# Optimization experiments

Hardware: AMD Instinct MI355X
Metric: run time of the kernel (lower is better)

The kernel has to match this reference:

```python
import jax, jax.numpy as jnp
import numpy as np

N = 8192      # nodes; also input feature dim (x.shape[0] used as in_channels)
E = 524288    # edges per edge type (avg degree 64)
H = 200       # hidden dim (hard-coded in RecomNet)
MEAN_RATING = 3.5


def setup_inputs() -> dict:
    key = jax.random.key(0)
    ks = jax.random.split(key, 14)
    s_in = np.float32(1.0 / np.sqrt(N))
    s_h = np.float32(1.0 / np.sqrt(H))
    return {
        "x": jax.random.normal(ks[0], (N, N), jnp.float32),
        "edge_sim": jax.random.randint(ks[1], (2, E), 0, N),
        "edge_rat": jax.random.randint(ks[2], (2, E), 0, N),
        "mask": jax.random.randint(ks[3], (E,), 0, 2).astype(bool),
        # conv1 params (in=N, out=H)
        "w1_self": jax.random.normal(ks[4], (N, H), jnp.float32) * s_in,
        "w1_sim": jax.random.normal(ks[5], (N, H), jnp.float32) * s_in,
        "w1_rat": jax.random.normal(ks[6], (N, H), jnp.float32) * s_in,
        "b1": jnp.zeros((H,), jnp.float32),
        # conv2 params (in=H, out=H)
        "w2_self": jax.random.normal(ks[7], (H, H), jnp.float32) * s_h,
        "w2_sim": jax.random.normal(ks[8], (H, H), jnp.float32) * s_h,
        "w2_rat": jax.random.normal(ks[9], (H, H), jnp.float32) * s_h,
        "b2": jnp.zeros((H,), jnp.float32),
        # bilinear decoder
        "Q": jax.random.normal(ks[10], (H, H), jnp.float32) * s_h,
    }


def _recom_conv(edge_sim, edge_rat, x, w_self, w_sim, w_rat, b):
    # linear-then-gather-then-scatter (linear commutes with sum aggregation)
    m_sim = (x @ w_sim)[edge_sim[0]]                                   # [E, H]
    agg_sim = jax.ops.segment_sum(m_sim, edge_sim[1], num_segments=N)  # [N, H]
    m_rat = (x @ w_rat)[edge_rat[0]]
    agg_rat = jax.ops.segment_sum(m_rat, edge_rat[1], num_segments=N)
    return x @ w_self + agg_sim + agg_rat + b


def reference(x, w1_self, w1_sim, w1_rat, b1, w2_self, w2_sim, w2_rat, b2, Q,
              edge_sim, edge_rat, mask):
    h = _recom_conv(edge_sim, edge_rat, x, w1_self, w1_sim, w1_rat, b1)
    h = jax.nn.relu(h)
    h = _recom_conv(edge_sim, edge_rat, h, w2_self, w2_sim, w2_rat, b2)
    h1 = h[edge_rat[0]]                                                # [E, H]
    h2 = h[edge_rat[1]]                                                # [E, H]
    pred = jnp.einsum("eh,hk,ek->e", h1, Q, h2) + MEAN_RATING          # [E]
    # original compacts with boolean mask (dynamic shape); here we keep a
    # fixed [E] output and zero out unmasked edges
    return jnp.where(mask, pred, 0.0)
```

## Files before the change

### kernel.cpp

```cpp
#include <hip/hip_runtime.h>

#define NN 8192
#define EE 524288
#define HPAD 256
#define NP 640
#define PSS ((size_t)NN * 200)
#define PSM ((size_t)NN * 400)

using s16x8 = __attribute__((ext_vector_type(8))) short;
using u16x8 = __attribute__((ext_vector_type(8))) unsigned short;
using f32x4 = __attribute__((ext_vector_type(4))) float;

__device__ __forceinline__ unsigned short f2b(float f) {
    unsigned u = __float_as_uint(f);
    u = (u + 0x7FFFu + ((u >> 16) & 1u)) >> 16;
    return (unsigned short)u;
}
__device__ __forceinline__ float b2f(unsigned short u) {
    return __uint_as_float((unsigned)u << 16);
}

__device__ __forceinline__ void async16(const unsigned short* g, unsigned short* l)
{
    __builtin_amdgcn_global_load_lds(
        (const __attribute__((address_space(1))) unsigned int*)g,
        (__attribute__((address_space(3))) unsigned int*)l, 16, 0, 0);
}


__global__ void cvt_f2b_kernel(const float* __restrict__ in,
                               unsigned short* __restrict__ out, int n8)
{
    int i = blockIdx.x * 256 + threadIdx.x;
    if (i >= n8) return;
    float4 v0 = ((const float4*)in)[2 * i];
    float4 v1 = ((const float4*)in)[2 * i + 1];
    u16x8 o;
    o[0] = f2b(v0.x); o[1] = f2b(v0.y); o[2] = f2b(v0.z); o[3] = f2b(v0.w);
    o[4] = f2b(v1.x); o[5] = f2b(v1.y); o[6] = f2b(v1.z); o[7] = f2b(v1.w);
    ((u16x8*)out)[i] = o;
}

__global__ void transpose_w_kernel(
    const float* __restrict__ u0, const float* __restrict__ u1,
    const float* __restrict__ u2,
    const float* __restrict__ v0, const float* __restrict__ v1,
    const float* __restrict__ v2,
    const float* __restrict__ Q,
    unsigned short* __restrict__ o0, unsigned short* __restrict__ o1,
    unsigned short* __restrict__ o2)
{
    const int zc = blockIdx.z;
    const float *w0, *w1, *w2;
    unsigned short* out;
    int Kout, Kreal, Nreal;
    if (zc == 0)      { w0 = u0; w1 = u1; w2 = u2; out = o0; Kout = NN;   Kreal = NN;  Nreal = 600; }
    else if (zc == 1) { w0 = v0; w1 = v1; w2 = v2; out = o1; Kout = HPAD; Kreal = 200; Nreal = 600; }
    else              { w0 = Q;  w1 = Q;  w2 = Q;  out = o2; Kout = HPAD; Kreal = 200; Nreal = 200; }
    const int kb = blockIdx.x << 5;
    const int nb = blockIdx.y << 5;
    if (kb >= Kout) return;
    __shared__ float tile[32][33];
    const int tx = threadIdx.x, ty = threadIdx.y;
    const int n = nb + tx;
    const float* w = (n < 200) ? w0 : (n < 400) ? w1 : w2;
    const int c = (n < 200) ? n : (n < 400) ? n - 200 : n - 400;
#pragma unroll
    for (int i = 0; i < 4; ++i) {
        const int k = kb + ty + (i << 3);
        float v = 0.f;
        if (n < Nreal && k < Kreal) v = w[(size_t)k * 200 + c];
        tile[ty + (i << 3)][tx] = v;
    }
    __syncthreads();
#pragma unroll
    for (int i = 0; i < 4; ++i) {
        const int nn = nb + ty + (i << 3);
        out[(size_t)nn * Kout + kb + tx] = f2b(tile[tx][ty + (i << 3)]);
    }
}

__global__ __launch_bounds__(256) void gemm_mfma(
    const unsigned short* __restrict__ A,
    const unsigned short* __restrict__ BT,
    int lda, int KC,
    unsigned short* __restrict__ Cb, int ldc,
    float* __restrict__ ys, unsigned short* __restrict__ ysb,
    unsigned short* __restrict__ yrb,
    float* __restrict__ ysp, unsigned short* __restrict__ ymp)
{
    __shared__ unsigned short As[2][128 * 64];
    __shared__ unsigned short Bs[2][128 * 64];
    const int tid  = threadIdx.x;
    const int lane = tid & 63;
    const int w    = tid >> 6;

    const int nx   = gridDim.x;
    const int flat = blockIdx.y * nx + blockIdx.x;
    const int cpx  = (nx * gridDim.y) >> 3;
    const int orig = (flat & 7) * cpx + (flat >> 3);
    const int by   = orig / nx;
    const int bx   = orig - by * nx;

    const int row0 = by << 7;
    const int col0 = bx << 7;
    const int z    = blockIdx.z;
    const int wm = (w >> 1) << 6;
    const int wn = (w & 1) << 6;

    const int sr = lane >> 3;
    const int sc = (lane & 7) ^ sr;
    const size_t kbase = (size_t)z * KC + ((size_t)sc << 3);
    const unsigned short* aG = A  + (size_t)(row0 + w * 8 + sr) * lda + kbase;
    const unsigned short* bG = BT + (size_t)(col0 + w * 8 + sr) * lda + kbase;
    const int ldsOff = w * 8;

    const f32x4 zero = {0.f, 0.f, 0.f, 0.f};
    f32x4 acc[4][4];
#pragma unroll
    for (int i = 0; i < 4; ++i)
#pragma unroll
        for (int j = 0; j < 4; ++j) acc[i][j] = zero;

#pragma unroll
    for (int it = 0; it < 4; ++it) {
        async16(aG + (size_t)(it * 32) * lda, &As[0][(it * 32 + ldsOff) << 6]);
        async16(bG + (size_t)(it * 32) * lda, &Bs[0][(it * 32 + ldsOff) << 6]);
    }
    __syncthreads();

    const int T = KC >> 6;
    for (int t = 0; t < T; ++t) {
        const int cur = t & 1;
        if (t + 1 < T) {
            const int ko = (t + 1) << 6;
#pragma unroll
            for (int it = 0; it < 4; ++it) {
                async16(aG + (size_t)(it * 32) * lda + ko,
                        &As[cur ^ 1][(it * 32 + ldsOff) << 6]);
                async16(bG + (size_t)(it * 32) * lda + ko,
                        &Bs[cur ^ 1][(it * 32 + ldsOff) << 6]);
            }
        }
#pragma unroll
        for (int kk = 0; kk < 2; ++kk) {
            const int q  = (kk << 2) + (lane >> 4);
            const int sl = (q ^ (lane & 7)) << 3;
            s16x8 af[4], bfv[4];
#pragma unroll
            for (int i = 0; i < 4; ++i) {
                const int rm = wm + (i << 4) + (lane & 15);
                af[i]  = *(const s16x8*)(&As[cur][(rm << 6) + sl]);
                const int rn = wn + (i << 4) + (lane & 15);
                bfv[i] = *(const s16x8*)(&Bs[cur][(rn << 6) + sl]);
            }
#pragma unroll
            for (int i = 0; i < 4; ++i)
#pragma unroll
                for (int j = 0; j < 4; ++j)
                    acc[i][j] = __builtin_amdgcn_mfma_f32_16x16x32_bf16(
                        af[i], bfv[j], acc[i][j], 0, 0, 0);
        }
        __syncthreads();
    }

    const int cr = (lane >> 4) << 2;
    const int cc = lane & 15;
    if (ymp) {
        float* sp = ysp + (size_t)z * PSS;
        unsigned short* mp = ymp + (size_t)z * PSM;
#pragma unroll
        for (int i = 0; i < 4; ++i)
#pragma unroll
            for (int j = 0; j < 4; ++j)
#pragma unroll
                for (int r = 0; r < 4; ++r) {
                    const int n = row0 + wm + (i << 4) + cr + r;
                    const int c = col0 + wn + (j << 4) + cc;
                    const float v = acc[i][j][r];
                    if (c < 200)      sp[(size_t)n * 200 + c] = v;
                    else if (c < 600) mp[(size_t)n * 400 + (c - 200)] = f2b(v);
                }
    } else if (ysb) {
#pragma unroll
        for (int i = 0; i < 4; ++i)
#pragma unroll
            for (int j = 0; j < 4; ++j)
#pragma unroll
                for (int r = 0; r < 4; ++r) {
                    const int n = row0 + wm + (i << 4) + cr + r;
                    const int c = col0 + wn + (j << 4) + cc;
                    const float v = acc[i][j][r];
                    if (c < 200)      ys [(size_t)n * 200 + c]        = v;
                    else if (c < 400) ysb[(size_t)n * 200 + (c - 200)] = f2b(v);
                    else if (c < 600) yrb[(size_t)n * 200 + (c - 400)] = f2b(v);
                }
    } else {
#pragma unroll
        for (int i = 0; i < 4; ++i)
#pragma unroll
            for (int j = 0; j < 4; ++j)
#pragma unroll
                for (int r = 0; r < 4; ++r)
                    Cb[(size_t)(row0 + wm + (i << 4) + cr + r) * ldc
                       + (col0 + wn + (j << 4) + cc)] = f2b(acc[i][j][r]);
    }
}

__global__ void combine_kernel(const float* __restrict__ ysp,
                               const unsigned short* __restrict__ ymp,
                               float* __restrict__ y_self,
                               unsigned short* __restrict__ y_simb,
                               unsigned short* __restrict__ y_ratb)
{
    int t = blockIdx.x * 256 + threadIdx.x;
    int n = t / 50, j4 = (t - n * 50) << 2;
    float4 s = {0.f, 0.f, 0.f, 0.f};
    float4 m = {0.f, 0.f, 0.f, 0.f};
    float4 r = {0.f, 0.f, 0.f, 0.f};
#pragma unroll
    for (int z = 0; z < 4; ++z) {
        float4 s2 = *(const float4*)(ysp + z * PSS + (size_t)n * 200 + j4);
        ushort4 m2 = *(const ushort4*)(ymp + z * PSM + (size_t)n * 400 + j4);
        ushort4 r2 = *(const ushort4*)(ymp + z * PSM + (size_t)n * 400 + 200 + j4);
        s.x += s2.x; s.y += s2.y; s.z += s2.z; s.w += s2.w;
        m.x += b2f(m2.x); m.y += b2f(m2.y); m.z += b2f(m2.z); m.w += b2f(m2.w);
        r.x += b2f(r2.x); r.y += b2f(r2.y); r.z += b2f(r2.z); r.w += b2f(r2.w);
    }
    *(float4*)(y_self + (size_t)n * 200 + j4) = s;
    ushort4 mo, ro;
    mo.x = f2b(m.x); mo.y = f2b(m.y); mo.z = f2b(m.z); mo.w = f2b(m.w);
    ro.x = f2b(r.x); ro.y = f2b(r.y); ro.z = f2b(r.z); ro.w = f2b(r.w);
    *(ushort4*)(y_simb + (size_t)n * 200 + j4) = mo;
    *(ushort4*)(y_ratb + (size_t)n * 200 + j4) = ro;
}


__global__ void hist_kernel(const int* __restrict__ e0, const int* __restrict__ e1,
                            int* __restrict__ d0, int* __restrict__ d1)
{
    const int* edges = blockIdx.y ? e1 : e0;
    int* deg = blockIdx.y ? d1 : d0;
    int e = blockIdx.x * 256 + threadIdx.x;
    if (e < EE) atomicAdd(&deg[edges[EE + e]], 1);
}

__global__ void scan_kernel(const int* __restrict__ deg0, int* __restrict__ off0,
                            int* __restrict__ pos0,
                            const int* __restrict__ deg1, int* __restrict__ off1,
                            int* __restrict__ pos1)
{
    const int* deg = blockIdx.x ? deg1 : deg0;
    int* off = blockIdx.x ? off1 : off0;
    int* pos = blockIdx.x ? pos1 : pos0;
    __shared__ int part[256];
    const int t = threadIdx.x;
    const int base = t * 32;
    int s = 0;
#pragma unroll
    for (int i = 0; i < 32; ++i) s += deg[base + i];
    part[t] = s;
    __syncthreads();
    for (int d = 1; d < 256; d <<= 1) {
        int v = (t >= d) ? part[t - d] : 0;
        __syncthreads();
        part[t] += v;
        __syncthreads();
    }
    int run = (t == 0) ? 0 : part[t - 1];
    for (int i = 0; i < 32; ++i) {
        off[base + i] = run;
        pos[base + i] = run;
        run += deg[base + i];
    }
    if (t == 255) off[NN] = run;
}

__global__ void reorder_kernel(const int* __restrict__ e0, int* __restrict__ pos0,
                               int2* __restrict__ se0,
                               const int* __restrict__ e1, int* __restrict__ pos1,
                               int2* __restrict__ se1)
{
    const int* edges = blockIdx.y ? e1 : e0;
    int* pos = blockIdx.y ? pos1 : pos0;
    int2* se = blockIdx.y ? se1 : se0;
    int e = blockIdx.x * 256 + threadIdx.x;
    if (e >= EE) return;
    int p = atomicAdd(&pos[edges[EE + e]], 1);
    se[p] = make_int2(edges[e], e);
}


__device__ __forceinline__ void edge_accum(
    const unsigned short* __restrict__ msg,
    const int* __restrict__ off, const int2* __restrict__ se,
    int n, int w, int j4, bool act, float4& acc)
{
    const int e1 = off[n + 1];
    int i = off[n] + w;
    for (; i + 12 < e1; i += 16) {
        const int s0 = se[i].x;
        const int s1 = se[i + 4].x;
        const int s2 = se[i + 8].x;
        const int s3 = se[i + 12].x;
        if (act) {
            ushort4 v0 = *(const ushort4*)(msg + (size_t)s0 * 200 + j4);
            ushort4 v1 = *(const ushort4*)(msg + (size_t)s1 * 200 + j4);
            ushort4 v2 = *(const ushort4*)(msg + (size_t)s2 * 200 + j4);
            ushort4 v3 = *(const ushort4*)(msg + (size_t)s3 * 200 + j4);
            acc.x += (b2f(v0.x) + b2f(v1.x)) + (b2f(v2.x) + b2f(v3.x));
            acc.y += (b2f(v0.y) + b2f(v1.y)) + (b2f(v2.y) + b2f(v3.y));
            acc.z += (b2f(v0.z) + b2f(v1.z)) + (b2f(v2.z) + b2f(v3.z));
            acc.w += (b2f(v0.w) + b2f(v1.w)) + (b2f(v2.w) + b2f(v3.w));
        }
    }
    for (; i < e1; i += 4) {
        const int s = se[i].x;
        if (act) {
            ushort4 v = *(const ushort4*)(msg + (size_t)s * 200 + j4);
            acc.x += b2f(v.x); acc.y += b2f(v.y);
            acc.z += b2f(v.z); acc.w += b2f(v.w);
        }
    }
}

__global__ __launch_bounds__(256) void agg_fused_kernel(
    const unsigned short* __restrict__ msg_sim,
    const unsigned short* __restrict__ msg_rat,
    const int* __restrict__ off_sim, const int2* __restrict__ se_sim,
    const int* __restrict__ off_rat, const int2* __restrict__ se_rat,
    const float* __restrict__ y_self, const float* __restrict__ bias,
    unsigned short* __restrict__ hb, int relu)
{
    __shared__ float part[4][200];
    const int n = blockIdx.x;
    const int w = threadIdx.x >> 6;
    const int lane = threadIdx.x & 63;
    const int j4 = lane << 2;
    const bool act = lane < 50;

    float4 acc = {0.f, 0.f, 0.f, 0.f};
    edge_accum(msg_sim, off_sim, se_sim, n, w, j4, act, acc);
    edge_accum(msg_rat, off_rat, se_rat, n, w, j4, act, acc);

    if (act) *(float4*)&part[w][j4] = acc;
    __syncthreads();
    const int j = threadIdx.x;
    if (j < 200) {
        float v = part[0][j] + part[1][j] + part[2][j] + part[3][j]
                + y_self[(size_t)n * 200 + j] + bias[j];
        if (relu) v = fmaxf(v, 0.f);
        hb[((size_t)n << 8) + j] = f2b(v);
    } else if (j < HPAD) {
        hb[((size_t)n << 8) + j] = 0;
    }
}

__global__ __launch_bounds__(256) void pred_kernel(
    const unsigned short* __restrict__ hQb,
    const unsigned short* __restrict__ h2b,
    const int* __restrict__ off, const int2* __restrict__ se,
    const int* __restrict__ mask, float* __restrict__ out)
{
    const int n = blockIdx.x;
    const int w = threadIdx.x >> 6;
    const int lane = threadIdx.x & 63;
    float4 b = {0.f, 0.f, 0.f, 0.f};
    if (lane < 50) {
        ushort4 v = *(const ushort4*)(h2b + ((size_t)n << 8) + (lane << 2));
        b.x = b2f(v.x); b.y = b2f(v.y); b.z = b2f(v.z); b.w = b2f(v.w);
    }
    const int e1 = off[n + 1];
    int i = off[n] + w;
    for (; i + 12 < e1; i += 16) {
        const int2 p0 = se[i];
        const int2 p1 = se[i + 4];
        const int2 p2 = se[i + 8];
        const int2 p3 = se[i + 12];
        float s0 = 0.f, s1 = 0.f, s2 = 0.f, s3 = 0.f;
        if (lane < 50) {
            ushort4 a0 = *(const ushort4*)(hQb + ((size_t)p0.x << 8) + (lane << 2));
            ushort4 a1 = *(const ushort4*)(hQb + ((size_t)p1.x << 8) + (lane << 2));
            ushort4 a2 = *(const ushort4*)(hQb + ((size_t)p2.x << 8) + (lane << 2));
            ushort4 a3 = *(const ushort4*)(hQb + ((size_t)p3.x << 8) + (lane << 2));
            s0 = fmaf(b2f(a0.x), b.x, fmaf(b2f(a0.y), b.y,
                 fmaf(b2f(a0.z), b.z, b2f(a0.w) * b.w)));
            s1 = fmaf(b2f(a1.x), b.x, fmaf(b2f(a1.y), b.y,
                 fmaf(b2f(a1.z), b.z, b2f(a1.w) * b.w)));
            s2 = fmaf(b2f(a2.x), b.x, fmaf(b2f(a2.y), b.y,
                 fmaf(b2f(a2.z), b.z, b2f(a2.w) * b.w)));
            s3 = fmaf(b2f(a3.x), b.x, fmaf(b2f(a3.y), b.y,
                 fmaf(b2f(a3.z), b.z, b2f(a3.w) * b.w)));
        }
#pragma unroll
        for (int o = 32; o > 0; o >>= 1) {
            s0 += __shfl_down(s0, o, 64);
            s1 += __shfl_down(s1, o, 64);
            s2 += __shfl_down(s2, o, 64);
            s3 += __shfl_down(s3, o, 64);
        }
        if (lane == 0) {
            out[p0.y] = mask[p0.y] ? (s0 + 3.5f) : 0.f;
            out[p1.y] = mask[p1.y] ? (s1 + 3.5f) : 0.f;
            out[p2.y] = mask[p2.y] ? (s2 + 3.5f) : 0.f;
            out[p3.y] = mask[p3.y] ? (s3 + 3.5f) : 0.f;
        }
    }
    for (; i < e1; i += 4) {
        const int2 p = se[i];
        float s = 0.f;
        if (lane < 50) {
            ushort4 a = *(const ushort4*)(hQb + ((size_t)p.x << 8) + (lane << 2));
            s = fmaf(b2f(a.x), b.x, fmaf(b2f(a.y), b.y,
                fmaf(b2f(a.z), b.z, b2f(a.w) * b.w)));
        }
#pragma unroll
        for (int o = 32; o > 0; o >>= 1) s += __shfl_down(s, o, 64);
        if (lane == 0) out[p.y] = mask[p.y] ? (s + 3.5f) : 0.f;
    }
}

extern "C" void kernel_launch(void* const* d_in, const int* in_sizes, int n_in,
                              void* d_out, int out_size, void* d_ws, size_t ws_size,
                              hipStream_t stream)
{
    const float* x       = (const float*)d_in[0];
    const int*   e_sim   = (const int*)d_in[1];
    const int*   e_rat   = (const int*)d_in[2];
    const int*   mask    = (const int*)d_in[3];
    const float* w1_self = (const float*)d_in[4];
    const float* w1_sim  = (const float*)d_in[5];
    const float* w1_rat  = (const float*)d_in[6];
    const float* b1      = (const float*)d_in[7];
    const float* w2_self = (const float*)d_in[8];
    const float* w2_sim  = (const float*)d_in[9];
    const float* w2_rat  = (const float*)d_in[10];
    const float* b2      = (const float*)d_in[11];
    const float* Q       = (const float*)d_in[12];
    float* out = (float*)d_out;

    char* p = (char*)d_ws;
    auto alloc = [&](size_t bytes) -> char* {
        char* r = p;
        p += (bytes + 255) & ~(size_t)255;
        return r;
    };
    unsigned short* xb    = (unsigned short*)alloc((size_t)NN * NN * 2);
    unsigned short* wbT1  = (unsigned short*)alloc((size_t)NP * NN * 2);
    unsigned short* wbT2  = (unsigned short*)alloc((size_t)NP * HPAD * 2);
    unsigned short* QT    = (unsigned short*)alloc((size_t)HPAD * HPAD * 2);
    float* ypart_s = (float*)alloc(4 * PSS * 4);
    unsigned short* ypart_m = (unsigned short*)alloc(4 * PSM * 2);
    float* y_self = (float*)alloc((size_t)NN * 200 * 4);
    unsigned short* y_simb = (unsigned short*)alloc((size_t)NN * 200 * 2);
    unsigned short* y_ratb = (unsigned short*)alloc((size_t)NN * 200 * 2);
    unsigned short* h1b = (unsigned short*)alloc((size_t)NN * HPAD * 2);
    unsigned short* h2b = (unsigned short*)alloc((size_t)NN * HPAD * 2);
    unsigned short* hQb = (unsigned short*)alloc((size_t)NN * HPAD * 2);
    int* deg_sim = (int*)alloc(NN * 4);
    int* deg_rat = (int*)alloc(NN * 4);
    int* off_sim = (int*)alloc((NN + 1) * 4);
    int* off_rat = (int*)alloc((NN + 1) * 4);
    int* pos_sim = (int*)alloc(NN * 4);
    int* pos_rat = (int*)alloc(NN * 4);
    int2* se_sim = (int2*)alloc((size_t)EE * 8);
    int2* se_rat = (int2*)alloc((size_t)EE * 8);

    const dim3 blk(256);
    const dim3 tblk(32, 8);

    cvt_f2b_kernel<<<(NN * NN / 8) / 256, blk, 0, stream>>>(x, xb, NN * NN / 8);
    transpose_w_kernel<<<dim3(NN / 32, NP / 32, 3), tblk, 0, stream>>>(
        w1_self, w1_sim, w1_rat, w2_self, w2_sim, w2_rat, Q, wbT1, wbT2, QT);

    hipMemsetAsync(deg_sim, 0, 2 * NN * 4, stream);
    hist_kernel<<<dim3(EE / 256, 2), blk, 0, stream>>>(e_sim, e_rat, deg_sim, deg_rat);
    scan_kernel<<<2, blk, 0, stream>>>(deg_sim, off_sim, pos_sim,
                                       deg_rat, off_rat, pos_rat);
    reorder_kernel<<<dim3(EE / 256, 2), blk, 0, stream>>>(
        e_sim, pos_sim, se_sim, e_rat, pos_rat, se_rat);

    gemm_mfma<<<dim3(NP / 128, NN / 128, 4), blk, 0, stream>>>(
        xb, wbT1, NN, NN / 4, nullptr, 0,
        nullptr, nullptr, nullptr, ypart_s, ypart_m);
    combine_kernel<<<NN * 50 / 256, blk, 0, stream>>>(
        ypart_s, ypart_m, y_self, y_simb, y_ratb);
    agg_fused_kernel<<<NN, blk, 0, stream>>>(
        y_simb, y_ratb, off_sim, se_sim, off_rat, se_rat, y_self, b1, h1b, 1);

    gemm_mfma<<<dim3(NP / 128, NN / 128, 1), blk, 0, stream>>>(
        h1b, wbT2, HPAD, HPAD, nullptr, 0,
        y_self, y_simb, y_ratb, nullptr, nullptr);
    agg_fused_kernel<<<NN, blk, 0, stream>>>(
        y_simb, y_ratb, off_sim, se_sim, off_rat, se_rat, y_self, b2, h2b, 0);

    gemm_mfma<<<dim3(HPAD / 128, NN / 128, 1), blk, 0, stream>>>(
        h2b, QT, HPAD, HPAD, hQb, HPAD,
        nullptr, nullptr, nullptr, nullptr, nullptr);
    pred_kernel<<<NN, blk, 0, stream>>>(hQb, h2b, off_rat, se_rat, mask, out);
}
```

Before: 833.6 us.

## Fuse fp32-to-bf16 conversion of x into the first GEMM's A-tile loads

Removes the separate pass that converts the 8192x8192 fp32 input to bf16. The first GEMM now loads fp32 rows of x into registers, converts them with packed bf16 instructions and writes the swizzled bf16 tile into LDS, overlapping this with the MFMA work of the current stage. This avoids writing and re-reading a 128 MB bf16 copy. In exchange, each GEMM block reads fp32 A data, and since five column blocks share each row tile, x is read several times at double width. The register-staged path also replaces async direct-to-LDS loads and adds VGPR pressure.

```diff
diff --git a/kernel.cpp b/kernel.cpp
--- a/kernel.cpp
+++ b/kernel.cpp
@@ -19,26 +19,17 @@
 __device__ __forceinline__ float b2f(unsigned short u) {
     return __uint_as_float((unsigned)u << 16);
 }
+__device__ __forceinline__ unsigned pkbf16(float a, float b) {
+    unsigned r;
+    asm("v_cvt_pk_bf16_f32 %0, %1, %2" : "=v"(r) : "v"(a), "v"(b));
+    return r;
+}
 
 __device__ __forceinline__ void async16(const unsigned short* g, unsigned short* l)
 {
     __builtin_amdgcn_global_load_lds(
         (const __attribute__((address_space(1))) unsigned int*)g,
         (__attribute__((address_space(3))) unsigned int*)l, 16, 0, 0);
-}
-
-
-__global__ void cvt_f2b_kernel(const float* __restrict__ in,
-                               unsigned short* __restrict__ out, int n8)
-{
-    int i = blockIdx.x * 256 + threadIdx.x;
-    if (i >= n8) return;
-    float4 v0 = ((const float4*)in)[2 * i];
-    float4 v1 = ((const float4*)in)[2 * i + 1];
-    u16x8 o;
-    o[0] = f2b(v0.x); o[1] = f2b(v0.y); o[2] = f2b(v0.z); o[3] = f2b(v0.w);
-    o[4] = f2b(v1.x); o[5] = f2b(v1.y); o[6] = f2b(v1.z); o[7] = f2b(v1.w);
-    ((u16x8*)out)[i] = o;
 }
 
 __global__ void transpose_w_kernel(
@@ -80,8 +71,9 @@
     }
 }
 
+template<int AF32>
 __global__ __launch_bounds__(256) void gemm_mfma(
-    const unsigned short* __restrict__ A,
+    const void* __restrict__ Araw,
     const unsigned short* __restrict__ BT,
     int lda, int KC,
     unsigned short* __restrict__ Cb, int ldc,
@@ -111,10 +103,22 @@
     const int sr = lane >> 3;
     const int sc = (lane & 7) ^ sr;
     const size_t kbase = (size_t)z * KC + ((size_t)sc << 3);
-    const unsigned short* aG = A  + (size_t)(row0 + w * 8 + sr) * lda + kbase;
     const unsigned short* bG = BT + (size_t)(col0 + w * 8 + sr) * lda + kbase;
     const int ldsOff = w * 8;
 
+    const unsigned short* aG = nullptr;
+    const float* aF = nullptr;
+    int ar = 0, aq = 0;
+    if constexpr (AF32) {
+        ar = (w << 5) + (lane >> 2);
+        aq = lane & 3;
+        aF = (const float*)Araw
+           + (size_t)(row0 + ar) * lda + (size_t)z * KC + aq * 16;
+    } else {
+        aG = (const unsigned short*)Araw
+           + (size_t)(row0 + w * 8 + sr) * lda + kbase;
+    }
+
     const f32x4 zero = {0.f, 0.f, 0.f, 0.f};
     f32x4 acc[4][4];
 #pragma unroll
@@ -122,25 +126,65 @@
 #pragma unroll
         for (int j = 0; j < 4; ++j) acc[i][j] = zero;
 
-#pragma unroll
-    for (int it = 0; it < 4; ++it) {
-        async16(aG + (size_t)(it * 32) * lda, &As[0][(it * 32 + ldsOff) << 6]);
-        async16(bG + (size_t)(it * 32) * lda, &Bs[0][(it * 32 + ldsOff) << 6]);
+    if constexpr (AF32) {
+        float4 lv[8];
+#pragma unroll
+        for (int p_ = 0; p_ < 2; ++p_) {
+            const float4* s4 = (const float4*)(aF + (size_t)(p_ * 16) * lda);
+#pragma unroll
+            for (int u = 0; u < 4; ++u) lv[p_ * 4 + u] = s4[u];
+        }
+#pragma unroll
+        for (int it = 0; it < 4; ++it)
+            async16(bG + (size_t)(it * 32) * lda, &Bs[0][(it * 32 + ldsOff) << 6]);
+#pragma unroll
+        for (int p_ = 0; p_ < 2; ++p_) {
+            const int r = ar + p_ * 16;
+            unsigned short* dst = &As[0][r << 6];
+#pragma unroll
+            for (int d = 0; d < 2; ++d) {
+                const int cch = aq * 2 + d;
+                const int sl  = cch ^ (r & 7);
+                const float4 x0 = lv[p_ * 4 + d * 2];
+                const float4 x1 = lv[p_ * 4 + d * 2 + 1];
+                uint4 o;
+                o.x = pkbf16(x0.x, x0.y); o.y = pkbf16(x0.z, x0.w);
+                o.z = pkbf16(x1.x, x1.y); o.w = pkbf16(x1.z, x1.w);
+                *(uint4*)(dst + (sl << 3)) = o;
+            }
+        }
+    } else {
+#pragma unroll
+        for (int it = 0; it < 4; ++it) {
+            async16(aG + (size_t)(it * 32) * lda, &As[0][(it * 32 + ldsOff) << 6]);
+            async16(bG + (size_t)(it * 32) * lda, &Bs[0][(it * 32 + ldsOff) << 6]);
+        }
     }
     __syncthreads();
 
     const int T = KC >> 6;
     for (int t = 0; t < T; ++t) {
         const int cur = t & 1;
+        float4 lv[8];
         if (t + 1 < T) {
             const int ko = (t + 1) << 6;
-#pragma unroll
-            for (int it = 0; it < 4; ++it) {
-                async16(aG + (size_t)(it * 32) * lda + ko,
-                        &As[cur ^ 1][(it * 32 + ldsOff) << 6]);
+            if constexpr (AF32) {
+#pragma unroll
+                for (int p_ = 0; p_ < 2; ++p_) {
+                    const float4* s4 = (const float4*)(aF + (size_t)(p_ * 16) * lda + ko);
+#pragma unroll
+                    for (int u = 0; u < 4; ++u) lv[p_ * 4 + u] = s4[u];
+                }
+            } else {
+#pragma unroll
+                for (int it = 0; it < 4; ++it)
+                    async16(aG + (size_t)(it * 32) * lda + ko,
+                            &As[cur ^ 1][(it * 32 + ldsOff) << 6]);
+            }
+#pragma unroll
+            for (int it = 0; it < 4; ++it)
                 async16(bG + (size_t)(it * 32) * lda + ko,
                         &Bs[cur ^ 1][(it * 32 + ldsOff) << 6]);
-            }
         }
 #pragma unroll
         for (int kk = 0; kk < 2; ++kk) {
@@ -160,6 +204,26 @@
                 for (int j = 0; j < 4; ++j)
                     acc[i][j] = __builtin_amdgcn_mfma_f32_16x16x32_bf16(
                         af[i], bfv[j], acc[i][j], 0, 0, 0);
+        }
+        if (t + 1 < T) {
+            if constexpr (AF32) {
+#pragma unroll
+                for (int p_ = 0; p_ < 2; ++p_) {
+                    const int r = ar + p_ * 16;
+                    unsigned short* dst = &As[cur ^ 1][r << 6];
+#pragma unroll
+                    for (int d = 0; d < 2; ++d) {
+                        const int cch = aq * 2 + d;
+                        const int sl  = cch ^ (r & 7);
+                        const float4 x0 = lv[p_ * 4 + d * 2];
+                        const float4 x1 = lv[p_ * 4 + d * 2 + 1];
+                        uint4 o;
+                        o.x = pkbf16(x0.x, x0.y); o.y = pkbf16(x0.z, x0.w);
+                        o.z = pkbf16(x1.x, x1.y); o.w = pkbf16(x1.z, x1.w);
+                        *(uint4*)(dst + (sl << 3)) = o;
+                    }
+                }
+            }
         }
         __syncthreads();
     }
@@ -445,7 +509,6 @@
         p += (bytes + 255) & ~(size_t)255;
         return r;
     };
-    unsigned short* xb    = (unsigned short*)alloc((size_t)NN * NN * 2);
     unsigned short* wbT1  = (unsigned short*)alloc((size_t)NP * NN * 2);
     unsigned short* wbT2  = (unsigned short*)alloc((size_t)NP * HPAD * 2);
     unsigned short* QT    = (unsigned short*)alloc((size_t)HPAD * HPAD * 2);
@@ -469,7 +532,6 @@
     const dim3 blk(256);
     const dim3 tblk(32, 8);
 
-    cvt_f2b_kernel<<<(NN * NN / 8) / 256, blk, 0, stream>>>(x, xb, NN * NN / 8);
     transpose_w_kernel<<<dim3(NN / 32, NP / 32, 3), tblk, 0, stream>>>(
         w1_self, w1_sim, w1_rat, w2_self, w2_sim, w2_rat, Q, wbT1, wbT2, QT);
 
@@ -480,21 +542,21 @@
     reorder_kernel<<<dim3(EE / 256, 2), blk, 0, stream>>>(
         e_sim, pos_sim, se_sim, e_rat, pos_rat, se_rat);
 
-    gemm_mfma<<<dim3(NP / 128, NN / 128, 4), blk, 0, stream>>>(
-        xb, wbT1, NN, NN / 4, nullptr, 0,
+    gemm_mfma<1><<<dim3(NP / 128, NN / 128, 4), blk, 0, stream>>>(
+        x, wbT1, NN, NN / 4, nullptr, 0,
         nullptr, nullptr, nullptr, ypart_s, ypart_m);
     combine_kernel<<<NN * 50 / 256, blk, 0, stream>>>(
         ypart_s, ypart_m, y_self, y_simb, y_ratb);
     agg_fused_kernel<<<NN, blk, 0, stream>>>(
         y_simb, y_ratb, off_sim, se_sim, off_rat, se_rat, y_self, b1, h1b, 1);
 
-    gemm_mfma<<<dim3(NP / 128, NN / 128, 1), blk, 0, stream>>>(
+    gemm_mfma<0><<<dim3(NP / 128, NN / 128, 1), blk, 0, stream>>>(
         h1b, wbT2, HPAD, HPAD, nullptr, 0,
         y_self, y_simb, y_ratb, nullptr, nullptr);
     agg_fused_kernel<<<NN, blk, 0, stream>>>(
         y_simb, y_ratb, off_sim, se_sim, off_rat, se_rat, y_self, b2, h2b, 0);
 
-    gemm_mfma<<<dim3(HPAD / 128, NN / 128, 1), blk, 0, stream>>>(
+    gemm_mfma<0><<<dim3(HPAD / 128, NN / 128, 1), blk, 0, stream>>>(
         h2b, QT, HPAD, HPAD, hQb, HPAD,
         nullptr, nullptr, nullptr, nullptr, nullptr);
     pred_kernel<<<NN, blk, 0, stream>>>(hQb, h2b, off_rat, se_rat, mask, out);
```

After: 803.0 us. -3.7%, faster.
